# Performance work log

Hardware: AMD Instinct MI355X
Metric: run time of the kernel (lower is better)

## Reference

```python
import jax, jax.numpy as jnp
import numpy as np

N_NODES = 100000
N_EDGES = 1000000
IN_FEAT = 64
OUT_FEAT = 64


def setup_inputs() -> dict:
    key = jax.random.key(0)
    ks = jax.random.split(key, 12)
    d, o = IN_FEAT, OUT_FEAT
    s = 1.0 / np.sqrt(d)
    s2 = 1.0 / np.sqrt(2 * d)
    return {
        "x": jax.random.normal(ks[0], (N_NODES, d), dtype=jnp.float32),
        "edge_index": jax.random.randint(ks[1], (2, N_EDGES), 0, N_NODES, dtype=jnp.int64),
        "batch": jnp.zeros((N_NODES,), dtype=jnp.int64),
        # message MLP: Linear(d,d) -> ReLU -> Linear(d,d)
        "msg_w1": jax.random.uniform(ks[2], (d, d), jnp.float32, -s, s),
        "msg_b1": jax.random.uniform(ks[3], (d,), jnp.float32, -s, s),
        "msg_w2": jax.random.uniform(ks[4], (d, d), jnp.float32, -s, s),
        "msg_b2": jax.random.uniform(ks[5], (d,), jnp.float32, -s, s),
        # output MLP: Linear(2d,d) -> ReLU -> Linear(d,out)
        "out_w1": jax.random.uniform(ks[6], (2 * d, d), jnp.float32, -s2, s2),
        "out_b1": jax.random.uniform(ks[7], (d,), jnp.float32, -s2, s2),
        "out_w2": jax.random.uniform(ks[8], (d, o), jnp.float32, -s, s),
        "out_b2": jax.random.uniform(ks[9], (o,), jnp.float32, -s, s),
    }


def reference(x, edge_index, batch, msg_w1, msg_b1, msg_w2, msg_b2,
              out_w1, out_b1, out_w2, out_b2):
    row, col = edge_index[0], edge_index[1]
    # gather source-node features per edge, apply message MLP
    h = x[row]                                   # [E, d]
    msg = jax.nn.relu(h @ msg_w1 + msg_b1) @ msg_w2 + msg_b2  # [E, d]
    # force processor: node features pass through as fx; scatter-sum messages
    fx = x                                        # [N, d]
    agg = jax.ops.segment_sum(msg, col, num_segments=N_NODES)  # [N, d]
    out_final = jnp.concatenate([fx, agg], axis=1)  # [N, 2d]
    out = jax.nn.relu(out_final @ out_w1 + out_b1) @ out_w2 + out_b2  # [N, out]
    return out
```

## Files before the change

### kernel.cpp

```cpp
#include <hip/hip_runtime.h>
#include <hip/hip_bf16.h>

#define D 64
#define BSHIFT 6
#define BW (1 << BSHIFT)
#define MAXB 2048
#define CAP 4096
#define STRIDE 2048
#define GT 256

typedef __attribute__((ext_vector_type(8))) short bf16x8;
typedef __attribute__((ext_vector_type(4))) float f32x4;

__device__ __forceinline__ short f2bf(float f) {
    __hip_bfloat16 h = __float2bfloat16(f);
    return *reinterpret_cast<short*>(&h);
}

__global__ __launch_bounds__(256) void msg_kernel(
    const float* __restrict__ x,
    const float* __restrict__ w1, const float* __restrict__ b1,
    const float* __restrict__ w2, const float* __restrict__ b2,
    __hip_bfloat16* __restrict__ m, int n_nodes)
{
    __shared__ __align__(16) __hip_bfloat16 sH[4][16 * 72];
    __shared__ short sW1[64 * 72];
    __shared__ short sW2[64 * 72];

    const int tid  = threadIdx.x;
    const int lane = tid & 63;
    const int wslot = tid >> 6;
    const int mr   = lane & 15;
    const int quad = lane >> 4;

    for (int i = tid; i < 1024; i += 256) {
        const int r = i >> 4, c = (i & 15) * 4;
        float4 f = *(const float4*)&w1[i * 4];
        short* d = &sW1[r * 72 + c];
        d[0] = f2bf(f.x); d[1] = f2bf(f.y); d[2] = f2bf(f.z); d[3] = f2bf(f.w);
        float4 g = *(const float4*)&w2[i * 4];
        short* e = &sW2[r * 72 + c];
        e[0] = f2bf(g.x); e[1] = f2bf(g.y); e[2] = f2bf(g.z); e[3] = f2bf(g.w);
    }
    __syncthreads();

    bf16x8 w1f[2][4], w2f[2][4];
    float  b1v[4], b2v[4];
#pragma unroll
    for (int ks = 0; ks < 2; ++ks)
#pragma unroll
        for (int nb = 0; nb < 4; ++nb) {
            bf16x8 f1, f2;
#pragma unroll
            for (int j = 0; j < 8; ++j) {
                int k = ks * 32 + quad * 8 + j;
                f1[j] = sW1[k * 72 + nb * 16 + mr];
                f2[j] = sW2[k * 72 + nb * 16 + mr];
            }
            w1f[ks][nb] = f1;
            w2f[ks][nb] = f2;
        }
#pragma unroll
    for (int nb = 0; nb < 4; ++nb) {
        b1v[nb] = b1[nb * 16 + mr];
        b2v[nb] = b2[nb * 16 + mr];
    }

    __hip_bfloat16* Hw = sH[wslot];
    const int wid    = (blockIdx.x * blockDim.x + threadIdx.x) >> 6;
    const int nwaves = (gridDim.x * blockDim.x) >> 6;
    const int ntiles = (n_nodes + 15) >> 4;

    for (int t = wid; t < ntiles; t += nwaves) {
        const int v0 = t * 16;
        int vr = v0 + mr;
        if (vr >= n_nodes) vr = n_nodes - 1;

        bf16x8 a[2];
#pragma unroll
        for (int ks = 0; ks < 2; ++ks) {
            const float* p = x + (size_t)vr * D + ks * 32 + quad * 8;
            float4 lo = *(const float4*)p;
            float4 hi = *(const float4*)(p + 4);
            bf16x8 f;
            f[0] = f2bf(lo.x); f[1] = f2bf(lo.y); f[2] = f2bf(lo.z); f[3] = f2bf(lo.w);
            f[4] = f2bf(hi.x); f[5] = f2bf(hi.y); f[6] = f2bf(hi.z); f[7] = f2bf(hi.w);
            a[ks] = f;
        }

#pragma unroll
        for (int nb = 0; nb < 4; ++nb) {
            f32x4 acc = {0.f, 0.f, 0.f, 0.f};
            acc = __builtin_amdgcn_mfma_f32_16x16x32_bf16(a[0], w1f[0][nb], acc, 0, 0, 0);
            acc = __builtin_amdgcn_mfma_f32_16x16x32_bf16(a[1], w1f[1][nb], acc, 0, 0, 0);
#pragma unroll
            for (int r = 0; r < 4; ++r) {
                float hv = fmaxf(acc[r] + b1v[nb], 0.f);
                Hw[(quad * 4 + r) * 72 + nb * 16 + mr] = __float2bfloat16(hv);
            }
        }

        bf16x8 h[2];
#pragma unroll
        for (int ks = 0; ks < 2; ++ks)
            h[ks] = *(const bf16x8*)&Hw[mr * 72 + ks * 32 + quad * 8];

#pragma unroll
        for (int nb = 0; nb < 4; ++nb) {
            f32x4 acc = {0.f, 0.f, 0.f, 0.f};
            acc = __builtin_amdgcn_mfma_f32_16x16x32_bf16(h[0], w2f[0][nb], acc, 0, 0, 0);
            acc = __builtin_amdgcn_mfma_f32_16x16x32_bf16(h[1], w2f[1][nb], acc, 0, 0, 0);
#pragma unroll
            for (int r = 0; r < 4; ++r)
                Hw[(quad * 4 + r) * 72 + nb * 16 + mr] =
                    __float2bfloat16(acc[r] + b2v[nb]);
        }

#pragma unroll
        for (int s = 0; s < 2; ++s) {
            const int rrow = s * 8 + (lane >> 3);
            const int cblk = (lane & 7) * 8;
            bf16x8 val = *(const bf16x8*)&Hw[rrow * 72 + cblk];
            const int vrow = v0 + rrow;
            if (vrow < n_nodes)
                *(bf16x8*)&m[(size_t)vrow * D + cblk] = val;
        }
    }
}

__global__ __launch_bounds__(256) void bin_kernel(
    const int* __restrict__ row, const int* __restrict__ col,
    int* __restrict__ gcur, unsigned int* __restrict__ tmp,
    int n_edges, int nbuckets, int chunk)
{
    __shared__ int hist[MAXB], base[MAXB], lcur[MAXB];
    const int t = threadIdx.x;
    const int e0 = blockIdx.x * chunk;
    const int e1 = min(e0 + chunk, n_edges);

    for (int i = t; i < nbuckets; i += 256) hist[i] = 0;
    __syncthreads();
    for (int e = e0 + t; e < e1; e += 256)
        atomicAdd(&hist[col[e] >> BSHIFT], 1);
    __syncthreads();
    for (int i = t; i < nbuckets; i += 256) {
        base[i] = hist[i] ? atomicAdd(&gcur[i], hist[i]) : 0;
        lcur[i] = 0;
    }
    __syncthreads();
    for (int e = e0 + t; e < e1; e += 256) {
        int c = col[e];
        int b = c >> BSHIFT;
        int loc = base[b] + atomicAdd(&lcur[b], 1);
        if (loc < STRIDE) {
            unsigned int val = ((unsigned int)(c & (BW - 1)) << 17)
                             | (unsigned int)row[e];
            tmp[(size_t)b * STRIDE + loc] = val;
        }
    }
}

__global__ __launch_bounds__(GT) void bucket_gather_kernel(
    const int* __restrict__ gcur, const unsigned int* __restrict__ tmp,
    const __hip_bfloat16* __restrict__ m, __hip_bfloat16* __restrict__ agg,
    int n_nodes, int nbuckets)
{
    __shared__ unsigned int sorted[CAP];
    __shared__ int cnt[BW], off[BW], cur[BW];

    const int b    = blockIdx.x;
    const int t    = threadIdx.x;
    const int lane = t & 63;
    const int wv   = t >> 6;
    const int vbase = b << BSHIFT;
    const unsigned int* gtmp = tmp + (size_t)b * STRIDE;

    const int total = min(gcur[b], STRIDE);

    float acc[16];
#pragma unroll
    for (int i = 0; i < 16; ++i) acc[i] = 0.f;

    for (int r0 = 0; r0 < total; r0 += CAP) {
        const int r1 = min(r0 + CAP, total);

        if (t < BW) cnt[t] = 0;
        __syncthreads();

        for (int i = r0 + t; i < r1; i += GT)
            atomicAdd(&cnt[gtmp[i] >> 17], 1);
        __syncthreads();

        if (wv == 0) {
            int a0 = cnt[lane];
            int s0 = a0;
#pragma unroll
            for (int d = 1; d < 64; d <<= 1) {
                int u0 = __shfl_up(s0, d, 64);
                if (lane >= d) s0 += u0;
            }
            const int e0 = s0 - a0;
            off[lane] = e0;
            cur[lane] = e0;
        }
        __syncthreads();

        for (int i = r0 + t; i < r1; i += GT) {
            unsigned int u = gtmp[i];
            int pos = atomicAdd(&cur[u >> 17], 1);
            sorted[pos] = u;
        }
        __syncthreads();

#pragma unroll
        for (int i = 0; i < 16; ++i) {
            const int n  = wv + (i << 2);
            const int o0 = off[n];
            const int c  = cnt[n];
            float s = 0.f;
            for (int cs = 0; cs < c; cs += 64) {
                const int k = min(64, c - cs);
                unsigned int pv = 0;
                if (lane < k) pv = sorted[o0 + cs + lane];

                int j = 0;
                for (; j + 8 <= k; j += 8) {
                    unsigned int u[8];
                    float v[8];
#pragma unroll
                    for (int q = 0; q < 8; ++q)
                        u[q] = __builtin_amdgcn_readlane(pv, j + q);
#pragma unroll
                    for (int q = 0; q < 8; ++q)
                        v[q] = (float)m[(size_t)(u[q] & 0x1FFFFu) * D + lane];
#pragma unroll
                    for (int q = 0; q < 8; ++q)
                        s += v[q];
                }
                for (; j < k; ++j) {
                    unsigned int u = __builtin_amdgcn_readlane(pv, j);
                    s += (float)m[(size_t)(u & 0x1FFFFu) * D + lane];
                }
            }
            acc[i] += s;
        }
        if (r1 < total) __syncthreads();
    }

#pragma unroll
    for (int i = 0; i < 16; ++i) {
        const int v = vbase + wv + (i << 2);
        if (v < n_nodes)
            agg[(size_t)v * D + lane] = __float2bfloat16(acc[i]);
    }
}

__global__ __launch_bounds__(256) void scatter_kernel(
    const int* __restrict__ row, const int* __restrict__ col,
    const __hip_bfloat16* __restrict__ m, float* __restrict__ aggf, int n_edges)
{
    const int lane = threadIdx.x & 63;
    const int wid  = (blockIdx.x * blockDim.x + threadIdx.x) >> 6;
    const int base = wid * 64;
    if (base >= n_edges) return;
    const int cnt = min(64, n_edges - base);

    int my_r = 0, my_c = 0;
    if (lane < cnt) { my_r = row[base + lane]; my_c = col[base + lane]; }

    for (int j = 0; j < cnt; ++j) {
        int r = __builtin_amdgcn_readlane(my_r, j);
        int c = __builtin_amdgcn_readlane(my_c, j);
        float v = (float)m[(size_t)r * D + lane];
        atomicAdd(&aggf[(size_t)c * D + lane], v);
    }
}

__global__ __launch_bounds__(256) void cvt_kernel(
    const float* __restrict__ aggf, __hip_bfloat16* __restrict__ agg, int n)
{
    int i = blockIdx.x * blockDim.x + threadIdx.x;
    if (i < n) agg[i] = __float2bfloat16(aggf[i]);
}

__global__ __launch_bounds__(256) void out_kernel(
    const float* __restrict__ x, const __hip_bfloat16* __restrict__ agg,
    const float* __restrict__ w1, const float* __restrict__ b1,
    const float* __restrict__ w2, const float* __restrict__ b2,
    float* __restrict__ out, int n_nodes)
{
    __shared__ __align__(16) __hip_bfloat16 sH[4][16 * 72];
    __shared__ short sW1[128 * 72];
    __shared__ short sW2[64 * 72];

    const int tid  = threadIdx.x;
    const int lane = tid & 63;
    const int wslot = tid >> 6;
    const int mr   = lane & 15;
    const int quad = lane >> 4;

    for (int i = tid; i < 2048; i += 256) {
        const int r = i >> 4, c = (i & 15) * 4;
        float4 f = *(const float4*)&w1[i * 4];
        short* d = &sW1[r * 72 + c];
        d[0] = f2bf(f.x); d[1] = f2bf(f.y); d[2] = f2bf(f.z); d[3] = f2bf(f.w);
    }
    for (int i = tid; i < 1024; i += 256) {
        const int r = i >> 4, c = (i & 15) * 4;
        float4 g = *(const float4*)&w2[i * 4];
        short* e = &sW2[r * 72 + c];
        e[0] = f2bf(g.x); e[1] = f2bf(g.y); e[2] = f2bf(g.z); e[3] = f2bf(g.w);
    }
    __syncthreads();

    bf16x8 w1f[4][4], w2f[2][4];
    float  b1v[4], b2v[4];
#pragma unroll
    for (int ks = 0; ks < 4; ++ks)
#pragma unroll
        for (int nb = 0; nb < 4; ++nb) {
            bf16x8 f;
#pragma unroll
            for (int j = 0; j < 8; ++j) {
                int k = ks * 32 + quad * 8 + j;
                f[j] = sW1[k * 72 + nb * 16 + mr];
            }
            w1f[ks][nb] = f;
        }
#pragma unroll
    for (int ks = 0; ks < 2; ++ks)
#pragma unroll
        for (int nb = 0; nb < 4; ++nb) {
            bf16x8 f;
#pragma unroll
            for (int j = 0; j < 8; ++j) {
                int k = ks * 32 + quad * 8 + j;
                f[j] = sW2[k * 72 + nb * 16 + mr];
            }
            w2f[ks][nb] = f;
        }
#pragma unroll
    for (int nb = 0; nb < 4; ++nb) {
        b1v[nb] = b1[nb * 16 + mr];
        b2v[nb] = b2[nb * 16 + mr];
    }

    __hip_bfloat16* Hw = sH[wslot];
    const int wid    = (blockIdx.x * blockDim.x + threadIdx.x) >> 6;
    const int nwaves = (gridDim.x * blockDim.x) >> 6;
    const int ntiles = (n_nodes + 15) >> 4;

    for (int t = wid; t < ntiles; t += nwaves) {
        const int v0 = t * 16;
        int vr = v0 + mr;
        if (vr >= n_nodes) vr = n_nodes - 1;

        bf16x8 a[4];
#pragma unroll
        for (int ks = 0; ks < 2; ++ks) {
            const float* p = x + (size_t)vr * D + ks * 32 + quad * 8;
            float4 lo = *(const float4*)p;
            float4 hi = *(const float4*)(p + 4);
            bf16x8 f;
            f[0] = f2bf(lo.x); f[1] = f2bf(lo.y); f[2] = f2bf(lo.z); f[3] = f2bf(lo.w);
            f[4] = f2bf(hi.x); f[5] = f2bf(hi.y); f[6] = f2bf(hi.z); f[7] = f2bf(hi.w);
            a[ks] = f;
        }
#pragma unroll
        for (int ks = 2; ks < 4; ++ks)
            a[ks] = *(const bf16x8*)&agg[(size_t)vr * D + (ks - 2) * 32 + quad * 8];

#pragma unroll
        for (int nb = 0; nb < 4; ++nb) {
            f32x4 acc = {0.f, 0.f, 0.f, 0.f};
#pragma unroll
            for (int ks = 0; ks < 4; ++ks)
                acc = __builtin_amdgcn_mfma_f32_16x16x32_bf16(a[ks], w1f[ks][nb], acc, 0, 0, 0);
#pragma unroll
            for (int r = 0; r < 4; ++r) {
                float hv = fmaxf(acc[r] + b1v[nb], 0.f);
                Hw[(quad * 4 + r) * 72 + nb * 16 + mr] = __float2bfloat16(hv);
            }
        }

        bf16x8 h[2];
#pragma unroll
        for (int ks = 0; ks < 2; ++ks)
            h[ks] = *(const bf16x8*)&Hw[mr * 72 + ks * 32 + quad * 8];

#pragma unroll
        for (int nb = 0; nb < 4; ++nb) {
            f32x4 acc = {0.f, 0.f, 0.f, 0.f};
            acc = __builtin_amdgcn_mfma_f32_16x16x32_bf16(h[0], w2f[0][nb], acc, 0, 0, 0);
            acc = __builtin_amdgcn_mfma_f32_16x16x32_bf16(h[1], w2f[1][nb], acc, 0, 0, 0);
#pragma unroll
            for (int r = 0; r < 4; ++r) {
                int vrow = v0 + quad * 4 + r;
                if (vrow < n_nodes)
                    out[(size_t)vrow * D + nb * 16 + mr] = acc[r] + b2v[nb];
            }
        }
    }
}

extern "C" void kernel_launch(void* const* d_in, const int* in_sizes, int n_in,
                              void* d_out, int out_size, void* d_ws, size_t ws_size,
                              hipStream_t stream) {
    const float* x   = (const float*)d_in[0];
    const int*   ei  = (const int*)d_in[1];
    const float* mw1 = (const float*)d_in[3];
    const float* mb1 = (const float*)d_in[4];
    const float* mw2 = (const float*)d_in[5];
    const float* mb2 = (const float*)d_in[6];
    const float* ow1 = (const float*)d_in[7];
    const float* ob1 = (const float*)d_in[8];
    const float* ow2 = (const float*)d_in[9];
    const float* ob2 = (const float*)d_in[10];

    const int n_nodes = in_sizes[0] / D;
    const int n_edges = in_sizes[1] / 2;
    const int* row = ei;
    const int* col = ei + n_edges;

    const int nbuckets = (n_nodes + BW - 1) >> BSHIFT;

    __hip_bfloat16* m   = (__hip_bfloat16*)d_ws;
    __hip_bfloat16* agg = m + (size_t)n_nodes * D;
    unsigned int* tmp   = (unsigned int*)(agg + (size_t)n_nodes * D);
    const size_t region = (size_t)nbuckets * STRIDE * 4 > (size_t)n_nodes * D * 4
                        ? (size_t)nbuckets * STRIDE * 4 : (size_t)n_nodes * D * 4;
    int* gcur = (int*)((char*)tmp + region);
    float* aggf = (float*)tmp;
    const size_t need = (size_t)n_nodes * D * 4 + region + (size_t)nbuckets * 4;

    const int ntiles = (n_nodes + 15) / 16;
    int nblk = (ntiles + 3) / 4;
    if (nblk > 512) nblk = 512;

    msg_kernel<<<nblk, 256, 0, stream>>>(x, mw1, mb1, mw2, mb2, m, n_nodes);

    const bool shape_ok = (n_nodes < (1 << 17)) && (nbuckets <= MAXB)
                       && (n_edges <= nbuckets * (STRIDE / 2));

    if (ws_size >= need && shape_ok) {
        hipMemsetAsync(gcur, 0, (size_t)nbuckets * sizeof(int), stream);
        const int nbbin = 256;
        const int chunk = (n_edges + nbbin - 1) / nbbin;
        bin_kernel<<<nbbin, 256, 0, stream>>>(row, col, gcur, tmp,
                                              n_edges, nbuckets, chunk);
        bucket_gather_kernel<<<nbuckets, GT, 0, stream>>>(gcur, tmp, m, agg,
                                                          n_nodes, nbuckets);
    } else {
        hipMemsetAsync(aggf, 0, (size_t)n_nodes * D * sizeof(float), stream);
        const int nwaves_s = (n_edges + 63) / 64;
        scatter_kernel<<<(nwaves_s + 3) / 4, 256, 0, stream>>>(row, col, m, aggf, n_edges);
        cvt_kernel<<<((n_nodes * D) + 255) / 256, 256, 0, stream>>>(aggf, agg, n_nodes * D);
    }

    out_kernel<<<nblk, 256, 0, stream>>>(x, agg, ow1, ob1, ow2, ob2,
                                         (float*)d_out, n_nodes);
}
```

Measured before the change: 188.5 us.

## Merge message MLP and edge binning into one heterogeneous launch

The per-node message MLP kernel and the edge-binning kernel are combined into a single launch. The first nmsg blocks run the MLP and the remaining blocks run binning, with a shared-memory buffer reused by both roles. Because the two phases are independent, they can run at the same time on the GPU, and one kernel launch boundary and its serialization are removed. The trade-off is that the block-level branch raises shared-memory use to the larger of the two roles, which may lower occupancy for the MLP blocks.

Result: faster. 181.7 us (-3.6%).

```diff
diff --git a/kernel.cpp b/kernel.cpp
--- a/kernel.cpp
+++ b/kernel.cpp
@@ -8,6 +8,7 @@
 #define CAP 4096
 #define STRIDE 2048
 #define GT 256
+#define SMEM_BYTES 27648
 
 typedef __attribute__((ext_vector_type(8))) short bf16x8;
 typedef __attribute__((ext_vector_type(4))) float f32x4;
@@ -17,15 +18,52 @@
     return *reinterpret_cast<short*>(&h);
 }
 
-__global__ __launch_bounds__(256) void msg_kernel(
+__global__ __launch_bounds__(256) void msg_bin_kernel(
     const float* __restrict__ x,
     const float* __restrict__ w1, const float* __restrict__ b1,
     const float* __restrict__ w2, const float* __restrict__ b2,
-    __hip_bfloat16* __restrict__ m, int n_nodes)
+    __hip_bfloat16* __restrict__ m, int n_nodes,
+    const int* __restrict__ row, const int* __restrict__ col,
+    int* __restrict__ gcur, unsigned int* __restrict__ tmp,
+    int n_edges, int nbuckets, int chunk, int nmsg)
 {
-    __shared__ __align__(16) __hip_bfloat16 sH[4][16 * 72];
-    __shared__ short sW1[64 * 72];
-    __shared__ short sW2[64 * 72];
+    __shared__ __align__(16) char smem[SMEM_BYTES];
+
+    if ((int)blockIdx.x >= nmsg) {
+        int* hist = (int*)smem;
+        int* base = hist + MAXB;
+        int* lcur = base + MAXB;
+        const int t = threadIdx.x;
+        const int bb = blockIdx.x - nmsg;
+        const int e0 = bb * chunk;
+        const int e1 = min(e0 + chunk, n_edges);
+
+        for (int i = t; i < nbuckets; i += 256) hist[i] = 0;
+        __syncthreads();
+        for (int e = e0 + t; e < e1; e += 256)
+            atomicAdd(&hist[col[e] >> BSHIFT], 1);
+        __syncthreads();
+        for (int i = t; i < nbuckets; i += 256) {
+            base[i] = hist[i] ? atomicAdd(&gcur[i], hist[i]) : 0;
+            lcur[i] = 0;
+        }
+        __syncthreads();
+        for (int e = e0 + t; e < e1; e += 256) {
+            int c = col[e];
+            int b = c >> BSHIFT;
+            int loc = base[b] + atomicAdd(&lcur[b], 1);
+            if (loc < STRIDE) {
+                unsigned int val = ((unsigned int)(c & (BW - 1)) << 17)
+                                 | (unsigned int)row[e];
+                tmp[(size_t)b * STRIDE + loc] = val;
+            }
+        }
+        return;
+    }
+
+    __hip_bfloat16* sHb = (__hip_bfloat16*)smem;
+    short* sW1 = (short*)(smem + 9216);
+    short* sW2 = (short*)(smem + 18432);
 
     const int tid  = threadIdx.x;
     const int lane = tid & 63;
@@ -66,9 +104,9 @@
         b2v[nb] = b2[nb * 16 + mr];
     }
 
-    __hip_bfloat16* Hw = sH[wslot];
-    const int wid    = (blockIdx.x * blockDim.x + threadIdx.x) >> 6;
-    const int nwaves = (gridDim.x * blockDim.x) >> 6;
+    __hip_bfloat16* Hw = sHb + wslot * (16 * 72);
+    const int wid    = (blockIdx.x * 256 + threadIdx.x) >> 6;
+    const int nwaves = nmsg * 4;
     const int ntiles = (n_nodes + 15) >> 4;
 
     for (int t = wid; t < ntiles; t += nwaves) {
@@ -124,38 +162,6 @@
             const int vrow = v0 + rrow;
             if (vrow < n_nodes)
                 *(bf16x8*)&m[(size_t)vrow * D + cblk] = val;
-        }
-    }
-}
-
-__global__ __launch_bounds__(256) void bin_kernel(
-    const int* __restrict__ row, const int* __restrict__ col,
-    int* __restrict__ gcur, unsigned int* __restrict__ tmp,
-    int n_edges, int nbuckets, int chunk)
-{
-    __shared__ int hist[MAXB], base[MAXB], lcur[MAXB];
-    const int t = threadIdx.x;
-    const int e0 = blockIdx.x * chunk;
-    const int e1 = min(e0 + chunk, n_edges);
-
-    for (int i = t; i < nbuckets; i += 256) hist[i] = 0;
-    __syncthreads();
-    for (int e = e0 + t; e < e1; e += 256)
-        atomicAdd(&hist[col[e] >> BSHIFT], 1);
-    __syncthreads();
-    for (int i = t; i < nbuckets; i += 256) {
-        base[i] = hist[i] ? atomicAdd(&gcur[i], hist[i]) : 0;
-        lcur[i] = 0;
-    }
-    __syncthreads();
-    for (int e = e0 + t; e < e1; e += 256) {
-        int c = col[e];
-        int b = c >> BSHIFT;
-        int loc = base[b] + atomicAdd(&lcur[b], 1);
-        if (loc < STRIDE) {
-            unsigned int val = ((unsigned int)(c & (BW - 1)) << 17)
-                             | (unsigned int)row[e];
-            tmp[(size_t)b * STRIDE + loc] = val;
         }
     }
 }
@@ -434,10 +440,8 @@
     const size_t need = (size_t)n_nodes * D * 4 + region + (size_t)nbuckets * 4;
 
     const int ntiles = (n_nodes + 15) / 16;
-    int nblk = (ntiles + 3) / 4;
-    if (nblk > 512) nblk = 512;
-
-    msg_kernel<<<nblk, 256, 0, stream>>>(x, mw1, mb1, mw2, mb2, m, n_nodes);
+    int nmsg = (ntiles + 3) / 4;
+    if (nmsg > 512) nmsg = 512;
 
     const bool shape_ok = (n_nodes < (1 << 17)) && (nbuckets <= MAXB)
                        && (n_edges <= nbuckets * (STRIDE / 2));
@@ -446,17 +450,21 @@
         hipMemsetAsync(gcur, 0, (size_t)nbuckets * sizeof(int), stream);
         const int nbbin = 256;
         const int chunk = (n_edges + nbbin - 1) / nbbin;
-        bin_kernel<<<nbbin, 256, 0, stream>>>(row, col, gcur, tmp,
-                                              n_edges, nbuckets, chunk);
+        msg_bin_kernel<<<nmsg + nbbin, 256, 0, stream>>>(
+            x, mw1, mb1, mw2, mb2, m, n_nodes,
+            row, col, gcur, tmp, n_edges, nbuckets, chunk, nmsg);
         bucket_gather_kernel<<<nbuckets, GT, 0, stream>>>(gcur, tmp, m, agg,
                                                           n_nodes, nbuckets);
     } else {
+        msg_bin_kernel<<<nmsg, 256, 0, stream>>>(
+            x, mw1, mb1, mw2, mb2, m, n_nodes,
+            row, col, gcur, tmp, n_edges, nbuckets, 0, nmsg);
         hipMemsetAsync(aggf, 0, (size_t)n_nodes * D * sizeof(float), stream);
         const int nwaves_s = (n_edges + 63) / 64;
         scatter_kernel<<<(nwaves_s + 3) / 4, 256, 0, stream>>>(row, col, m, aggf, n_edges);
         cvt_kernel<<<((n_nodes * D) + 255) / 256, 256, 0, stream>>>(aggf, agg, n_nodes * D);
     }
 
-    out_kernel<<<nblk, 256, 0, stream>>>(x, agg, ow1, ob1, ow2, ob2,
+    out_kernel<<<nmsg, 256, 0, stream>>>(x, agg, ow1, ob1, ow2, ob2,
                                          (float*)d_out, n_nodes);
 }
```
